# Kernel optimization log

Measured on AMD Instinct MI355X. Metric: run time of the kernel, lower is better.

Reference implementation:

```python
import jax, jax.numpy as jnp
import numpy as np

N_HEAD = 16
D_MODEL = 1024
HEAD_DIM = D_MODEL // N_HEAD  # 64
LAMBDA_INIT = 0.8 - 0.6 * float(np.exp(-0.3 * 1))  # layer_depth = 1


def setup_inputs() -> dict:
    key = jax.random.key(0)
    ks = jax.random.split(key, 10)
    B, T, D = 1, 2048, D_MODEL
    std = 0.02
    return {
        "x": jax.random.normal(ks[0], (B, T, D), jnp.float32),
        "Wq": jax.random.normal(ks[1], (D, D), jnp.float32) * std,
        "Wk": jax.random.normal(ks[2], (D, D), jnp.float32) * std,
        "Wv": jax.random.normal(ks[3], (D, D), jnp.float32) * std,
        "Wproj": jax.random.normal(ks[4], (D, D), jnp.float32) * std,
        "lambda_q1": jax.random.normal(ks[5], (HEAD_DIM // 2,), jnp.float32) * 0.1,
        "lambda_k1": jax.random.normal(ks[6], (HEAD_DIM // 2,), jnp.float32) * 0.1,
        "lambda_q2": jax.random.normal(ks[7], (HEAD_DIM // 2,), jnp.float32) * 0.1,
        "lambda_k2": jax.random.normal(ks[8], (HEAD_DIM // 2,), jnp.float32) * 0.1,
    }


def _rms_norm(x):
    # F.rms_norm with no weight: x / sqrt(mean(x^2) + eps)
    eps = jnp.finfo(x.dtype).eps
    return x * jax.lax.rsqrt(jnp.mean(jnp.square(x), axis=-1, keepdims=True) + eps)


def _rotary_cos_sin(T, dim, base=10000.0):
    inv_freq = 1.0 / (base ** (jnp.arange(0, dim, 2, dtype=jnp.float32) / dim))
    freqs = jnp.outer(jnp.arange(T, dtype=jnp.float32), inv_freq)  # [T, dim/2]
    return jnp.cos(freqs), jnp.sin(freqs)


def _apply_rotary(x, cos, sin):
    # x: [B, T, 2, H, hd]; cos/sin: [T, hd/2] broadcast over (group, head)
    d = x.shape[-1] // 2
    c = cos[None, :, None, None, :]
    s = sin[None, :, None, None, :]
    x1, x2 = x[..., :d], x[..., d:]
    return jnp.concatenate([x1 * c + x2 * s, -x1 * s + x2 * c], axis=-1)


def _causal_attn(q, k, v, scale):
    # q,k: [B, T, H, hd]; v: [B, T, H, dv] -> [B, T, H, dv]
    T = q.shape[1]
    scores = jnp.einsum("bthd,bshd->bhts", q, k) * scale  # [B,H,T,T]
    mask = jnp.tril(jnp.ones((T, T), dtype=bool))
    scores = jnp.where(mask, scores, -jnp.inf)
    w = jax.nn.softmax(scores, axis=-1)
    return jnp.einsum("bhts,bshd->bthd", w, v)


def reference(x, Wq, Wk, Wv, Wproj, lambda_q1, lambda_k1, lambda_q2, lambda_k2):
    B, T, D = x.shape
    nh, hd = N_HEAD, HEAD_DIM
    q = (x @ Wq.T).reshape(B, T, 2, nh // 2, hd)
    k = (x @ Wk.T).reshape(B, T, 2, nh // 2, hd)
    v = (x @ Wv.T).reshape(B, T, nh // 2, 2 * hd)

    q, k = _rms_norm(q), _rms_norm(k)
    cos, sin = _rotary_cos_sin(T, hd)
    q, k = _apply_rotary(q, cos, sin), _apply_rotary(k, cos, sin)

    q1, q2 = q[:, :, 0], q[:, :, 1]
    k1, k2 = k[:, :, 0], k[:, :, 1]

    scale = 1.0 / jnp.sqrt(jnp.asarray(hd, x.dtype))
    y1 = _causal_attn(q1, k1, v, scale)  # [B,T,nh/2,2*hd]
    y2 = _causal_attn(q2, k2, v, scale)

    lambda_1 = jnp.exp(jnp.sum(lambda_q1 * lambda_k1))
    lambda_2 = jnp.exp(jnp.sum(lambda_q2 * lambda_k2))
    lambda_full = lambda_1 - lambda_2 + LAMBDA_INIT

    y = (y1 - lambda_full * y2).reshape(B, T, D)
    return y @ Wproj.T
```

## Files before the change

### kernel.cpp

```cpp
#include <hip/hip_runtime.h>
#include <hip/hip_bf16.h>

typedef __attribute__((ext_vector_type(4))) float f32x4;
typedef __attribute__((ext_vector_type(8))) short bf16x8;
typedef unsigned short u16;

#define T_SEQ 2048
#define DMODEL 1024

__device__ __forceinline__ u16 f2bf(float f) {
    __hip_bfloat16 h = __float2bfloat16(f);
    return __builtin_bit_cast(unsigned short, h);
}
__device__ __forceinline__ u16 f2h(float f) {
    _Float16 h = (_Float16)f;
    return __builtin_bit_cast(unsigned short, h);
}
__device__ __forceinline__ float h2f(u16 b) {
    return (float)__builtin_bit_cast(_Float16, b);
}

typedef const void __attribute__((address_space(1))) gvoid_t;
typedef void __attribute__((address_space(3))) lvoid_t;
__device__ __forceinline__ void gload16(const void* g, void* l) {
    __builtin_amdgcn_global_load_lds((gvoid_t*)g, (lvoid_t*)l, 16, 0, 0);
}

__device__ __forceinline__ int swz(int row, int colb) {
    return colb ^ ((row & 7) << 4);
}

__device__ __forceinline__ void cast4(const float* __restrict__ s,
                                      u16* __restrict__ d, int u) {
    int i = u * 4;
    float4 v = *(const float4*)(s + i);
    ushort4 o;
    o.x = f2bf(v.x); o.y = f2bf(v.y); o.z = f2bf(v.z); o.w = f2bf(v.w);
    *(ushort4*)(d + i) = o;
}

__global__ __launch_bounds__(256) void prep(const float* __restrict__ x,
                                            const float* __restrict__ Wq,
                                            const float* __restrict__ Wk,
                                            const float* __restrict__ Wv,
                                            const float* __restrict__ Wp,
                                            u16* __restrict__ x_bf, u16* __restrict__ wq_bf,
                                            u16* __restrict__ wk_bf, u16* __restrict__ wv_bf,
                                            u16* __restrict__ wp_bf,
                                            float* __restrict__ cosT, float* __restrict__ sinT,
                                            const float* __restrict__ lq1, const float* __restrict__ lk1,
                                            const float* __restrict__ lq2, const float* __restrict__ lk2,
                                            float* __restrict__ lam) {
    int b = blockIdx.x;
    if (b < 6144) {
        int u = b * 256 + threadIdx.x;
        if (u < 524288)       cast4(x,  x_bf,  u);
        else if (u < 786432)  cast4(Wq, wq_bf, u - 524288);
        else if (u < 1048576) cast4(Wk, wk_bf, u - 786432);
        else if (u < 1310720) cast4(Wv, wv_bf, u - 1048576);
        else                  cast4(Wp, wp_bf, u - 1310720);
    } else if (b < 6400) {
        int i = (b - 6144) * 256 + threadIdx.x;
        int t = i >> 5, j = i & 31;
        float inv = powf(10000.0f, -(float)j * (1.0f / 32.0f));
        float fr = (float)t * inv;
        cosT[i] = cosf(fr);
        sinT[i] = sinf(fr);
    } else if (threadIdx.x == 0) {
        float s1 = 0.f, s2 = 0.f;
        for (int i = 0; i < 32; ++i) { s1 += lq1[i] * lk1[i]; s2 += lq2[i] * lk2[i]; }
        *lam = expf(s1) - expf(s2) + 0.35550906759096928f;
    }
}

__device__ __forceinline__ void gemm_main64(const u16* __restrict__ A,
                                            const u16* __restrict__ B,
                                            int m0, int n0, int K,
                                            u16* lA, u16* lB, f32x4 acc[2][4]) {
    const int tid = threadIdx.x;
    const int lane = tid & 63;
    const int wid = tid >> 6;
    const int wr = (wid >> 1) * 32;
    const int wc = (wid & 1) * 64;
    const int fr = lane & 15;
    const int kc = lane >> 4;
    const char* Ab = (const char*)A;
    const char* Bb = (const char*)B;
    const int rowbytes = K * 2;

    for (int k0 = 0; k0 < K; k0 += 32) {
        {
            int c = tid;
            gload16(Ab + (size_t)(m0 + (c >> 2)) * rowbytes + k0 * 2 + (c & 3) * 16,
                    (char*)lA + c * 16);
        }
#pragma unroll
        for (int i = 0; i < 2; ++i) {
            int c = i * 256 + tid;
            gload16(Bb + (size_t)(n0 + (c >> 2)) * rowbytes + k0 * 2 + (c & 3) * 16,
                    (char*)lB + c * 16);
        }
        __syncthreads();
        bf16x8 a[2], b[4];
#pragma unroll
        for (int m = 0; m < 2; ++m) a[m] = *(const bf16x8*)&lA[(wr + m * 16 + fr) * 32 + kc * 8];
#pragma unroll
        for (int n = 0; n < 4; ++n) b[n] = *(const bf16x8*)&lB[(wc + n * 16 + fr) * 32 + kc * 8];
#pragma unroll
        for (int m = 0; m < 2; ++m)
#pragma unroll
            for (int n = 0; n < 4; ++n)
                acc[m][n] = __builtin_amdgcn_mfma_f32_16x16x32_bf16(a[m], b[n], acc[m][n], 0, 0, 0);
        __syncthreads();
    }
}

__global__ __launch_bounds__(256) void gemm_qkv(const u16* __restrict__ A,
                                                const u16* __restrict__ wq,
                                                const u16* __restrict__ wk,
                                                const u16* __restrict__ wv,
                                                const float* __restrict__ cosT,
                                                const float* __restrict__ sinT,
                                                u16* __restrict__ q_bf,
                                                u16* __restrict__ k_bf,
                                                u16* __restrict__ Vbf) {
    __shared__ __align__(16) u16 lA[64 * 32];
    __shared__ __align__(16) u16 lB[128 * 32];
    const int nt = blockIdx.x;
    const int which = nt >> 3;
    const u16* B = (which == 0) ? wq : (which == 1) ? wk : wv;
    const int m0 = blockIdx.y * 64;
    const int n0 = (nt & 7) * 128;

    f32x4 acc[2][4] = {};
    gemm_main64(A, B, m0, n0, 1024, lA, lB, acc);

    const int lane = threadIdx.x & 63;
    const int wid = threadIdx.x >> 6;
    const int wr = (wid >> 1) * 32;
    const int wc = (wid & 1) * 64;
    const int fr = lane & 15;
    const int rr = (lane >> 4) * 4;

    if (which == 2) {
#pragma unroll
        for (int m = 0; m < 2; ++m)
#pragma unroll
            for (int n = 0; n < 4; ++n)
#pragma unroll
                for (int r = 0; r < 4; ++r)
                    Vbf[(size_t)(m0 + wr + m * 16 + rr + r) * 1024 + n0 + wc + n * 16 + fr] =
                        f2bf(acc[m][n][r]);
        return;
    }

    const int cb = n0 + wc;
    const int plane = ((cb >> 9) << 3) | ((cb >> 6) & 7);
    u16* dstp = ((which == 0) ? q_bf : k_bf) + (size_t)plane * T_SEQ * 64;
#pragma unroll
    for (int m = 0; m < 2; ++m)
#pragma unroll
        for (int r = 0; r < 4; ++r) {
            int t = m0 + wr + m * 16 + rr + r;
            float s2 = 0.f;
#pragma unroll
            for (int n = 0; n < 4; ++n) { float a = acc[m][n][r]; s2 += a * a; }
            s2 += __shfl_xor(s2, 1); s2 += __shfl_xor(s2, 2);
            s2 += __shfl_xor(s2, 4); s2 += __shfl_xor(s2, 8);
            float inv = rsqrtf(s2 * (1.0f / 64.0f) + 1.1920929e-7f);
#pragma unroll
            for (int n = 0; n < 4; ++n) {
                float a = acc[m][n][r] * inv;
                float p_ = acc[m][n ^ 2][r] * inv;
                int jj = ((n & 1) << 4) + fr;
                float c = cosT[t * 32 + jj], sn = sinT[t * 32 + jj];
                float ov = (n < 2) ? (a * c + p_ * sn) : (a * c - p_ * sn);
                dstp[(size_t)t * 64 + n * 16 + fr] = f2bf(ov);
            }
        }
}

__global__ __launch_bounds__(256) void gemm_proj(const u16* __restrict__ A,
                                                 const u16* __restrict__ B,
                                                 float* __restrict__ C) {
    __shared__ __align__(16) u16 lA[64 * 32];
    __shared__ __align__(16) u16 lB[128 * 32];
    const int m0 = blockIdx.y * 64;
    const int n0 = blockIdx.x * 128;
    f32x4 acc[2][4] = {};
    gemm_main64(A, B, m0, n0, 1024, lA, lB, acc);
    const int lane = threadIdx.x & 63;
    const int wid = threadIdx.x >> 6;
    const int wr = (wid >> 1) * 32;
    const int wc = (wid & 1) * 64;
    const int fr = lane & 15;
    const int rr = (lane >> 4) * 4;
#pragma unroll
    for (int m = 0; m < 2; ++m)
#pragma unroll
        for (int n = 0; n < 4; ++n)
#pragma unroll
            for (int r = 0; r < 4; ++r)
                C[(size_t)(m0 + wr + m * 16 + rr + r) * 1024 + (n0 + wc + n * 16 + fr)] =
                    acc[m][n][r];
}

__global__ __launch_bounds__(256) void vtrans(const u16* __restrict__ Vbf,
                                              u16* __restrict__ vT) {
    __shared__ u16 tile[32][34];
    int tx = threadIdx.x & 31;
    int ty = threadIdx.x >> 5;
    int c0 = blockIdx.x * 32;
    int r0 = blockIdx.y * 32;
#pragma unroll
    for (int i = ty; i < 32; i += 8)
        tile[i][tx] = Vbf[(size_t)(r0 + i) * 1024 + c0 + tx];
    __syncthreads();
#pragma unroll
    for (int i = ty; i < 32; i += 8)
        vT[(size_t)(c0 + i) * T_SEQ + r0 + tx] = tile[tx][i];
}

__global__ __launch_bounds__(512) void attn_kernel(const u16* __restrict__ q_bf,
                                                   const u16* __restrict__ k_bf,
                                                   const u16* __restrict__ vT_bf,
                                                   u16* __restrict__ Oc,
                                                   float2* __restrict__ ml) {
    __shared__ __align__(16) u16 lK[2][64 * 64];
    __shared__ __align__(16) u16 lV[2][128 * 64];
    __shared__ __align__(16) u16 lP[8][16 * 64];

    const int tid = threadIdx.x, lane = tid & 63, wid = tid >> 6;
    const int bid = blockIdx.x;
    const int plane = bid & 15;
    const int u = bid >> 4;
    int qt, chunk;
    if (u < 16)      { qt = 15 - (u >> 2);            chunk = u & 3; }
    else if (u < 28) { int w = u - 16; qt = 11 - w / 3; chunk = w % 3; }
    else if (u < 36) { int w = u - 28; qt = 7 - (w >> 1); chunk = w & 1; }
    else             { qt = 3 - (u - 36);             chunk = 0; }
    const int ntot = 2 * qt + 2;
    const int tb = chunk * 8;
    const int te = min(tb + 8, ntot);
    const int q0 = qt * 128;
    const int h = plane & 7;

    const u16* qp = q_bf + (size_t)plane * T_SEQ * 64;
    const char* kp = (const char*)(k_bf + (size_t)plane * T_SEQ * 64);
    const char* vp = (const char*)(vT_bf + (size_t)h * 128 * T_SEQ);
    const int fr = lane & 15, kc = lane >> 4;
    const int wsub = wid * 16;
    char* lPw = (char*)lP[wid];

    bf16x8 aq[2];
#pragma unroll
    for (int kq = 0; kq < 2; ++kq)
        aq[kq] = *(const bf16x8*)(qp + (size_t)(q0 + wsub + fr) * 64 + kq * 32 + kc * 8);

    f32x4 o[8] = {};
    float mi_l = -1e30f, li_l = 0.f;
    const float SL = 0.125f * 1.4426950408889634f;
    const int qrow = q0 + wsub + fr;

    auto stage = [&](int b, int t) {
        int s0 = t << 6;
        {
            int row = tid >> 3, cp = (tid & 7) * 16;
            gload16(kp + (size_t)(s0 + row) * 128 + swz(row, cp), (char*)lK[b] + tid * 16);
        }
#pragma unroll
        for (int i = 0; i < 2; ++i) {
            int c = i * 512 + tid;
            int row = c >> 3, cp = (c & 7) * 16;
            gload16(vp + (size_t)row * (T_SEQ * 2) + (size_t)s0 * 2 + swz(row, cp),
                    (char*)lV[b] + c * 16);
        }
    };

    auto compute = [&](const char* lKb, const char* lVb, int s0, bool diag) {
        f32x4 sacc[4] = {};
        __builtin_amdgcn_s_setprio(1);
#pragma unroll
        for (int kq = 0; kq < 2; ++kq)
#pragma unroll
            for (int n = 0; n < 4; ++n) {
                int row = n * 16 + fr;
                bf16x8 bk = *(const bf16x8*)(lKb + row * 128 + swz(row, kq * 64 + kc * 16));
                sacc[n] = __builtin_amdgcn_mfma_f32_16x16x32_bf16(bk, aq[kq], sacc[n], 0, 0, 0);
            }
        __builtin_amdgcn_s_setprio(0);

#pragma unroll
        for (int n = 0; n < 4; ++n)
#pragma unroll
            for (int r = 0; r < 4; ++r)
                sacc[n][r] *= SL;
        if (diag) {
#pragma unroll
            for (int n = 0; n < 4; ++n)
#pragma unroll
                for (int r = 0; r < 4; ++r)
                    if (s0 + n * 16 + kc * 4 + r > qrow) sacc[n][r] = -1e30f;
        }
        float rmax = -1e30f;
#pragma unroll
        for (int n = 0; n < 4; ++n)
#pragma unroll
            for (int r = 0; r < 4; ++r)
                rmax = fmaxf(rmax, sacc[n][r]);
        rmax = fmaxf(rmax, __shfl_xor(rmax, 16));
        rmax = fmaxf(rmax, __shfl_xor(rmax, 32));

        bool raise = rmax > mi_l + 8.0f;
        float f = raise ? __builtin_exp2f(mi_l - rmax) : 1.0f;
        if (raise) mi_l = rmax;

        float rs = 0.f;
#pragma unroll
        for (int n = 0; n < 4; ++n)
#pragma unroll
            for (int r = 0; r < 4; ++r) {
                float p = __builtin_exp2f(sacc[n][r] - mi_l);
                sacc[n][r] = p;
                rs += p;
            }
        rs += __shfl_xor(rs, 16);
        rs += __shfl_xor(rs, 32);
        li_l = li_l * f + rs;

        if (__any(raise)) {
#pragma unroll
            for (int n8 = 0; n8 < 8; ++n8)
#pragma unroll
                for (int r = 0; r < 4; ++r) o[n8][r] *= f;
        }

#pragma unroll
        for (int n = 0; n < 4; ++n) {
            ushort4 pk;
            pk.x = f2bf(sacc[n][0]); pk.y = f2bf(sacc[n][1]);
            pk.z = f2bf(sacc[n][2]); pk.w = f2bf(sacc[n][3]);
            *(ushort4*)(lPw + fr * 128 + ((n * 32 + kc * 8) ^ ((fr & 7) << 4))) = pk;
        }

        __builtin_amdgcn_s_setprio(1);
#pragma unroll
        for (int kk = 0; kk < 2; ++kk) {
            bf16x8 ap = *(const bf16x8*)(lPw + fr * 128 + swz(fr, kk * 64 + kc * 16));
#pragma unroll
            for (int n8 = 0; n8 < 8; ++n8) {
                int row = n8 * 16 + fr;
                bf16x8 bv = *(const bf16x8*)(lVb + row * 128 + swz(row, kk * 64 + kc * 16));
                o[n8] = __builtin_amdgcn_mfma_f32_16x16x32_bf16(bv, ap, o[n8], 0, 0, 0);
            }
        }
        __builtin_amdgcn_s_setprio(0);
    };

    stage(0, tb);
    for (int t = tb; t < te; ++t) {
        int ib = (t - tb) & 1;
        if (t + 1 < te) {
            stage(ib ^ 1, t + 1);
            asm volatile("s_waitcnt vmcnt(3)" ::: "memory");
        } else {
            asm volatile("s_waitcnt vmcnt(0)" ::: "memory");
        }
        __builtin_amdgcn_sched_barrier(0);
        __builtin_amdgcn_s_barrier();
        __builtin_amdgcn_sched_barrier(0);
        compute((const char*)lK[ib], (const char*)lV[ib], t << 6, t >= ntot - 2);
        __builtin_amdgcn_s_barrier();
    }

    const float inv_l = 1.0f / li_l;
    u16* Ob = Oc + ((size_t)(plane * 4 + chunk) * T_SEQ + qrow) * 128;
#pragma unroll
    for (int n8 = 0; n8 < 8; ++n8) {
        ushort4 w;
        w.x = f2h(o[n8][0] * inv_l);
        w.y = f2h(o[n8][1] * inv_l);
        w.z = f2h(o[n8][2] * inv_l);
        w.w = f2h(o[n8][3] * inv_l);
        *(ushort4*)(Ob + n8 * 16 + kc * 4) = w;
    }
    if (kc == 0)
        ml[(size_t)(plane * 4 + chunk) * T_SEQ + qrow] = make_float2(mi_l, li_l);
}

__global__ __launch_bounds__(256) void merge_kernel(const u16* __restrict__ Oc,
                                                    const float2* __restrict__ ml,
                                                    const float* __restrict__ lamp,
                                                    u16* __restrict__ yc) {
    int uu = blockIdx.x * 256 + threadIdx.x;
    int t = uu >> 8, rem = uu & 255, h = rem >> 5, d4 = (rem & 31) * 4;
    int qt = t >> 7;
    int nc = (qt + 4) >> 2;
    float lamv = *lamp;
    float yv[2][4];
#pragma unroll
    for (int v = 0; v < 2; ++v) {
        int plane = v * 8 + h;
        float2 m_l[4];
        float M = -1e30f;
#pragma unroll
        for (int c = 0; c < 4; ++c)
            if (c < nc) {
                m_l[c] = ml[(size_t)(plane * 4 + c) * T_SEQ + t];
                M = fmaxf(M, m_l[c].x);
            }
        float den = 0.f, a0 = 0.f, a1 = 0.f, a2 = 0.f, a3 = 0.f;
#pragma unroll
        for (int c = 0; c < 4; ++c)
            if (c < nc) {
                float w = __builtin_exp2f(m_l[c].x - M) * m_l[c].y;
                den += w;
                ushort4 ov = *(const ushort4*)(Oc +
                    ((size_t)(plane * 4 + c) * T_SEQ + t) * 128 + d4);
                a0 += w * h2f(ov.x);
                a1 += w * h2f(ov.y);
                a2 += w * h2f(ov.z);
                a3 += w * h2f(ov.w);
            }
        float inv = 1.0f / den;
        yv[v][0] = a0 * inv; yv[v][1] = a1 * inv;
        yv[v][2] = a2 * inv; yv[v][3] = a3 * inv;
    }
    ushort4 o;
    o.x = f2bf(yv[0][0] - lamv * yv[1][0]);
    o.y = f2bf(yv[0][1] - lamv * yv[1][1]);
    o.z = f2bf(yv[0][2] - lamv * yv[1][2]);
    o.w = f2bf(yv[0][3] - lamv * yv[1][3]);
    *(ushort4*)(yc + (size_t)t * 1024 + h * 128 + d4) = o;
}

extern "C" void kernel_launch(void* const* d_in, const int* in_sizes, int n_in,
                              void* d_out, int out_size, void* d_ws, size_t ws_size,
                              hipStream_t stream) {
    const float* x   = (const float*)d_in[0];
    const float* Wq  = (const float*)d_in[1];
    const float* Wk  = (const float*)d_in[2];
    const float* Wv  = (const float*)d_in[3];
    const float* Wp  = (const float*)d_in[4];
    const float* lq1 = (const float*)d_in[5];
    const float* lk1 = (const float*)d_in[6];
    const float* lq2 = (const float*)d_in[7];
    const float* lk2 = (const float*)d_in[8];
    float* out = (float*)d_out;

    char* ws = (char*)d_ws;
    u16*    x_bf  = (u16*)(ws);
    u16*    wq_bf = (u16*)(ws + (4ull << 20));
    u16*    wk_bf = (u16*)(ws + (6ull << 20));
    u16*    wv_bf = (u16*)(ws + (8ull << 20));
    u16*    wp_bf = (u16*)(ws + (10ull << 20));
    u16*    Vbf   = (u16*)(ws + (12ull << 20));
    u16*    q_bf  = (u16*)(ws + (16ull << 20));
    u16*    k_bf  = (u16*)(ws + (20ull << 20));
    u16*    vT_bf = (u16*)(ws + (24ull << 20));
    u16*    Oc    = (u16*)(ws + (28ull << 20));
    float2* ml    = (float2*)(ws + (60ull << 20));
    u16*    yc_bf = (u16*)(ws + (61ull << 20));
    float*  cosT  = (float*)(ws + (65ull << 20));
    float*  sinT  = (float*)(ws + (65ull << 20) + (256ull << 10));
    float*  lam   = (float*)(ws + (65ull << 20) + (512ull << 10));

    prep<<<6401, 256, 0, stream>>>(x, Wq, Wk, Wv, Wp,
                                   x_bf, wq_bf, wk_bf, wv_bf, wp_bf,
                                   cosT, sinT, lq1, lk1, lq2, lk2, lam);

    gemm_qkv<<<dim3(24, 32), 256, 0, stream>>>(x_bf, wq_bf, wk_bf, wv_bf,
                                               cosT, sinT, q_bf, k_bf, Vbf);

    vtrans<<<dim3(32, 64), 256, 0, stream>>>(Vbf, vT_bf);

    attn_kernel<<<640, 512, 0, stream>>>(q_bf, k_bf, vT_bf, Oc, ml);

    merge_kernel<<<2048, 256, 0, stream>>>(Oc, ml, lam, yc_bf);

    gemm_proj<<<dim3(8, 32), 256, 0, stream>>>(yc_bf, wp_bf, out);
}
```

Before: 112.1 us.

## Redistribute attention P via cross-lane shuffles instead of LDS; fold softmax scale into Q

```diff
diff --git a/kernel.cpp b/kernel.cpp
--- a/kernel.cpp
+++ b/kernel.cpp
@@ -4,6 +4,7 @@
 typedef __attribute__((ext_vector_type(4))) float f32x4;
 typedef __attribute__((ext_vector_type(8))) short bf16x8;
 typedef unsigned short u16;
+typedef unsigned int u32;
 
 #define T_SEQ 2048
 #define DMODEL 1024
@@ -154,6 +155,7 @@
         return;
     }
 
+    const float oscale = (which == 0) ? 0.18033688011112042f : 1.0f;
     const int cb = n0 + wc;
     const int plane = ((cb >> 9) << 3) | ((cb >> 6) & 7);
     u16* dstp = ((which == 0) ? q_bf : k_bf) + (size_t)plane * T_SEQ * 64;
@@ -175,7 +177,7 @@
                 int jj = ((n & 1) << 4) + fr;
                 float c = cosT[t * 32 + jj], sn = sinT[t * 32 + jj];
                 float ov = (n < 2) ? (a * c + p_ * sn) : (a * c - p_ * sn);
-                dstp[(size_t)t * 64 + n * 16 + fr] = f2bf(ov);
+                dstp[(size_t)t * 64 + n * 16 + fr] = f2bf(ov * oscale);
             }
         }
 }
@@ -221,14 +223,13 @@
         vT[(size_t)(c0 + i) * T_SEQ + r0 + tx] = tile[tx][i];
 }
 
-__global__ __launch_bounds__(512) void attn_kernel(const u16* __restrict__ q_bf,
-                                                   const u16* __restrict__ k_bf,
-                                                   const u16* __restrict__ vT_bf,
-                                                   u16* __restrict__ Oc,
-                                                   float2* __restrict__ ml) {
+__global__ __launch_bounds__(512, 6) void attn_kernel(const u16* __restrict__ q_bf,
+                                                      const u16* __restrict__ k_bf,
+                                                      const u16* __restrict__ vT_bf,
+                                                      u16* __restrict__ Oc,
+                                                      float2* __restrict__ ml) {
     __shared__ __align__(16) u16 lK[2][64 * 64];
     __shared__ __align__(16) u16 lV[2][128 * 64];
-    __shared__ __align__(16) u16 lP[8][16 * 64];
 
     const int tid = threadIdx.x, lane = tid & 63, wid = tid >> 6;
     const int bid = blockIdx.x;
@@ -250,7 +251,6 @@
     const char* vp = (const char*)(vT_bf + (size_t)h * 128 * T_SEQ);
     const int fr = lane & 15, kc = lane >> 4;
     const int wsub = wid * 16;
-    char* lPw = (char*)lP[wid];
 
     bf16x8 aq[2];
 #pragma unroll
@@ -259,8 +259,10 @@
 
     f32x4 o[8] = {};
     float mi_l = -1e30f, li_l = 0.f;
-    const float SL = 0.125f * 1.4426950408889634f;
     const int qrow = q0 + wsub + fr;
+    const int srcA = fr + ((kc & 1) << 5);
+    const int srcB = srcA + 16;
+    const bool hi = kc >= 2;
 
     auto stage = [&](int b, int t) {
         int s0 = t << 6;
@@ -290,11 +292,6 @@
             }
         __builtin_amdgcn_s_setprio(0);
 
-#pragma unroll
-        for (int n = 0; n < 4; ++n)
-#pragma unroll
-            for (int r = 0; r < 4; ++r)
-                sacc[n][r] *= SL;
         if (diag) {
 #pragma unroll
             for (int n = 0; n < 4; ++n)
@@ -335,23 +332,38 @@
                 for (int r = 0; r < 4; ++r) o[n8][r] *= f;
         }
 
-#pragma unroll
-        for (int n = 0; n < 4; ++n) {
-            ushort4 pk;
-            pk.x = f2bf(sacc[n][0]); pk.y = f2bf(sacc[n][1]);
-            pk.z = f2bf(sacc[n][2]); pk.w = f2bf(sacc[n][3]);
-            *(ushort4*)(lPw + fr * 128 + ((n * 32 + kc * 8) ^ ((fr & 7) << 4))) = pk;
-        }
+        u32 w32[4][2];
+#pragma unroll
+        for (int n = 0; n < 4; ++n)
+#pragma unroll
+            for (int w = 0; w < 2; ++w) {
+                u32 rpk;
+                asm("v_cvt_pk_bf16_f32 %0, %1, %2"
+                    : "=v"(rpk) : "v"(sacc[n][2 * w]), "v"(sacc[n][2 * w + 1]));
+                w32[n][w] = rpk;
+            }
 
         __builtin_amdgcn_s_setprio(1);
 #pragma unroll
         for (int kk = 0; kk < 2; ++kk) {
-            bf16x8 ap = *(const bf16x8*)(lPw + fr * 128 + swz(fr, kk * 64 + kc * 16));
+            u32 a0 = (u32)__shfl((int)w32[2 * kk][0], srcA);
+            u32 a1 = (u32)__shfl((int)w32[2 * kk][1], srcA);
+            u32 a2 = (u32)__shfl((int)w32[2 * kk][0], srcB);
+            u32 a3 = (u32)__shfl((int)w32[2 * kk][1], srcB);
+            u32 b0 = (u32)__shfl((int)w32[2 * kk + 1][0], srcA);
+            u32 b1 = (u32)__shfl((int)w32[2 * kk + 1][1], srcA);
+            u32 b2 = (u32)__shfl((int)w32[2 * kk + 1][0], srcB);
+            u32 b3 = (u32)__shfl((int)w32[2 * kk + 1][1], srcB);
+            union { u32 u4[4]; bf16x8 v; } ap;
+            ap.u4[0] = hi ? b0 : a0;
+            ap.u4[1] = hi ? b1 : a1;
+            ap.u4[2] = hi ? b2 : a2;
+            ap.u4[3] = hi ? b3 : a3;
 #pragma unroll
             for (int n8 = 0; n8 < 8; ++n8) {
                 int row = n8 * 16 + fr;
                 bf16x8 bv = *(const bf16x8*)(lVb + row * 128 + swz(row, kk * 64 + kc * 16));
-                o[n8] = __builtin_amdgcn_mfma_f32_16x16x32_bf16(bv, ap, o[n8], 0, 0, 0);
+                o[n8] = __builtin_amdgcn_mfma_f32_16x16x32_bf16(bv, ap.v, o[n8], 0, 0, 0);
             }
         }
         __builtin_amdgcn_s_setprio(0);
```

Result: no change. 110.8 us (-1.2%).
